# Kernel tuning notes

Hardware: AMD Instinct MI355X
Metric: run time of the kernel (lower is better)

## Reference

```python
import jax, jax.numpy as jnp
import numpy as np

NUM_USER = 100000
NUM_ITEM = 50000
DIM_E = 128
DIM_FEAT = 256
BATCH = 1024
NUM_NEG = 127
TEMP = 2.0
LR_LAMBDA = 0.5
NUM_SAMPLE = 0.5


def _l2norm(x, eps=1e-12):
    n = jnp.linalg.norm(x, axis=1, keepdims=True)
    return x / jnp.maximum(n, eps)


def setup_inputs() -> dict:
    key = jax.random.key(0)
    ks = jax.random.split(key, 9)
    flat = BATCH * (1 + NUM_NEG)
    user_tensor = jax.random.randint(ks[0], (BATCH, 1 + NUM_NEG), 0, NUM_USER, dtype=jnp.int64 if jax.config.jax_enable_x64 else jnp.int32)
    item_tensor = jax.random.randint(ks[1], (BATCH, 1 + NUM_NEG), NUM_USER, NUM_USER + NUM_ITEM, dtype=user_tensor.dtype)
    rand_index = jax.random.randint(ks[2], (int(flat * NUM_SAMPLE),), 0, flat, dtype=user_tensor.dtype)
    id_embedding = jax.random.normal(ks[3], (NUM_USER + NUM_ITEM, DIM_E), jnp.float32) * 0.02
    v_feat = jax.random.normal(ks[4], (NUM_ITEM, DIM_FEAT), jnp.float32)
    W1 = jax.random.normal(ks[5], (DIM_FEAT, 256), jnp.float32) * (1.0 / np.sqrt(DIM_FEAT))
    b1 = jax.random.normal(ks[6], (256,), jnp.float32) * 0.01
    W2 = jax.random.normal(ks[7], (256, DIM_E), jnp.float32) * (1.0 / 16.0)
    b2 = jax.random.normal(ks[8], (DIM_E,), jnp.float32) * 0.01
    return {"user_tensor": user_tensor, "item_tensor": item_tensor, "rand_index": rand_index,
            "id_embedding": id_embedding, "v_feat": v_feat, "W1": W1, "b1": b1, "W2": W2, "b2": b2}


def _contrastive(anchor, all_t):
    # exp(<a,b>/T) grouped into [B, 1+num_neg]; pos is column 0
    score = jnp.exp(jnp.sum(anchor * all_t, axis=1) / TEMP).reshape(-1, 1 + NUM_NEG)
    pos = score[:, 0]
    tot = jnp.sum(score, axis=1)
    return jnp.mean(-jnp.log(pos / tot))


def reference(user_tensor, item_tensor, rand_index, id_embedding, v_feat, W1, b1, W2, b2):
    # encoder: normalize content feats, 2-layer MLP
    feature = _l2norm(v_feat)
    feature = jax.nn.leaky_relu(feature @ W1 + b1)  # slope 0.01, matches torch default
    feature = feature @ W2 + b2                      # [num_item, dim_E]

    pos_flat = jnp.repeat(item_tensor[:, 0:1], 1 + NUM_NEG, axis=1).reshape(-1)
    u_flat = user_tensor.reshape(-1)
    i_flat = item_tensor.reshape(-1)

    all_item_feat = feature[i_flat - NUM_USER]          # [flat, dim_E]
    user_emb = id_embedding[u_flat]
    pos_emb = id_embedding[pos_flat]
    all_item_emb = id_embedding[i_flat]

    head_feat = _l2norm(all_item_feat)
    head_embed = _l2norm(pos_emb)

    # replace a random half of the item embeddings with content features
    all_item_input = all_item_emb.at[rand_index].set(all_item_feat[rand_index])

    c1 = _contrastive(head_embed, head_feat)
    c2 = _contrastive(user_emb, all_item_input)

    reg_loss = (jnp.mean(jnp.sqrt(jnp.sum(user_emb ** 2, axis=1))) +
                jnp.mean(jnp.sqrt(jnp.sum(all_item_emb ** 2, axis=1)))) / 2

    # graph_generator is None -> graph contrastive loss is 0
    total = c1 * LR_LAMBDA + c2 * (1.0 - LR_LAMBDA)
    return total, reg_loss
```

## Files before the change

kernel.cpp:

```cpp
#include <hip/hip_runtime.h>
#include <math.h>

#define NUSER 100000
#define NITEM 50000
#define NID   (NUSER + NITEM)
#define DIM_E 128
#define DIM_F 256
#define BATCH 1024
#define NCOL 128
#define FLAT (BATCH * NCOL)

typedef __attribute__((ext_vector_type(8))) short bf16x8;
typedef __attribute__((ext_vector_type(4))) short bf16x4;
typedef __attribute__((ext_vector_type(4))) float f32x4;

__device__ __forceinline__ float dot4(float4 a, float4 b) {
    return a.x * b.x + a.y * b.y + a.z * b.z + a.w * b.w;
}

__device__ __forceinline__ short f2bf(float x) {
    unsigned u = __float_as_uint(x);
    unsigned r = (u + 0x7FFFu + ((u >> 16) & 1u)) >> 16;
    return (short)r;
}

__device__ __forceinline__ float bf2f(short s) {
    return __uint_as_float(((unsigned)(unsigned short)s) << 16);
}

__global__ __launch_bounds__(256) void zero_flags_kernel(int* __restrict__ flags) {
    int i = blockIdx.x * 256 + threadIdx.x;
    if (i < FLAT) flags[i] = 0;
}

__global__ __launch_bounds__(256) void scatter_flags_kernel(const int* __restrict__ ridx,
                                                            int n, int* __restrict__ flags) {
    int i = blockIdx.x * 256 + threadIdx.x;
    if (i < n) flags[ridx[i]] = 1;
}

__global__ __launch_bounds__(256) void prep_kernel(const float* __restrict__ W1,
                                                   const float* __restrict__ W2,
                                                   short* __restrict__ w1t,
                                                   short* __restrict__ w2t) {
    int i = blockIdx.x * 256 + threadIdx.x;
    if (i < 256 * 256) {
        int n = i >> 8, k = i & 255;
        w1t[i] = f2bf(W1[(size_t)k * 256 + n]);
    } else if (i < 256 * 256 + 128 * 256) {
        int j = i - 256 * 256;
        int n = j >> 8, k = j & 255;
        w2t[j] = f2bf(W2[(size_t)k * 128 + n]);
    }
}

__global__ __launch_bounds__(256) void conv_kernel(const float* __restrict__ idemb,
                                                   short* __restrict__ idemb_bf,
                                                   float* __restrict__ norms) {
    const int sub = threadIdx.x & 31;
    const int g0 = (blockIdx.x * 256 + threadIdx.x) >> 5;
    const int ng = gridDim.x * 8;
    for (int row = g0; row < NID; row += ng) {
        float4 v = *(const float4*)(idemb + (size_t)row * DIM_E + sub * 4);
        float s = dot4(v, v);
#pragma unroll
        for (int off = 16; off >= 1; off >>= 1) s += __shfl_xor(s, off);
        bf16x4 p;
        p[0] = f2bf(v.x); p[1] = f2bf(v.y); p[2] = f2bf(v.z); p[3] = f2bf(v.w);
        *(bf16x4*)(idemb_bf + (size_t)row * DIM_E + sub * 4) = p;
        if (sub == 0) norms[row] = sqrtf(s);
    }
}

__device__ __forceinline__ void stage_rows(const float4 va[4], int srow, int q,
                                           short* __restrict__ As) {
    float s = 0.f;
#pragma unroll
    for (int c = 0; c < 4; ++c) s += dot4(va[c], va[c]);
#pragma unroll
    for (int off = 8; off >= 1; off >>= 1) s += __shfl_xor(s, off);
    float inv = 1.f / fmaxf(sqrtf(s), 1e-12f);
    bf16x8 p0, p1;
    p0[0] = f2bf(va[0].x * inv); p0[1] = f2bf(va[0].y * inv);
    p0[2] = f2bf(va[0].z * inv); p0[3] = f2bf(va[0].w * inv);
    p0[4] = f2bf(va[1].x * inv); p0[5] = f2bf(va[1].y * inv);
    p0[6] = f2bf(va[1].z * inv); p0[7] = f2bf(va[1].w * inv);
    p1[0] = f2bf(va[2].x * inv); p1[1] = f2bf(va[2].y * inv);
    p1[2] = f2bf(va[2].z * inv); p1[3] = f2bf(va[2].w * inv);
    p1[4] = f2bf(va[3].x * inv); p1[5] = f2bf(va[3].y * inv);
    p1[6] = f2bf(va[3].z * inv); p1[7] = f2bf(va[3].w * inv);
    const int sw = (srow & 7) << 3;
    *(bf16x8*)(&As[srow * 256 + ((q * 16) ^ sw)]) = p0;
    *(bf16x8*)(&As[srow * 256 + ((q * 16 + 8) ^ sw)]) = p1;
}

__global__ __launch_bounds__(512, 2) void mlp_mfma_kernel(const float* __restrict__ vfeat,
                                                          const short* __restrict__ w1t,
                                                          const float* __restrict__ b1,
                                                          const short* __restrict__ w2t,
                                                          const float* __restrict__ b2,
                                                          short* __restrict__ featout) {
    __shared__ __align__(16) short As[32 * 256];
    __shared__ __align__(16) short Hs[32 * 256];
    const int t = threadIdx.x;
    const int w = t >> 6;
    const int l = t & 63;
    const int fr = l & 15;
    const int kg = l >> 4;
    const int srow = t >> 4;
    const int q = t & 15;
    const int NT = (NITEM + 31) / 32;

    bf16x8 B1f[8][2];
    bf16x8 B2f[8];
#pragma unroll
    for (int kc = 0; kc < 8; ++kc) {
#pragma unroll
        for (int ct = 0; ct < 2; ++ct)
            B1f[kc][ct] = *(const bf16x8*)(w1t + (size_t)(w * 32 + ct * 16 + fr) * 256 + kc * 32 + kg * 8);
        B2f[kc] = *(const bf16x8*)(w2t + (size_t)(w * 16 + fr) * 256 + kc * 32 + kg * 8);
    }
    float b1v[2];
    b1v[0] = b1[w * 32 + fr];
    b1v[1] = b1[w * 32 + 16 + fr];
    const float b2v = b2[w * 16 + fr];

    int tile = blockIdx.x;
    {
        float4 va[4];
        int gr = tile * 32 + srow;
        const float* src = vfeat + (size_t)gr * DIM_F + q * 16;
#pragma unroll
        for (int c = 0; c < 4; ++c)
            va[c] = (gr < NITEM) ? *(const float4*)(src + c * 4) : make_float4(0.f, 0.f, 0.f, 0.f);
        stage_rows(va, srow, q, As);
    }
    __syncthreads();

    while (tile < NT) {
        const int tnext = tile + gridDim.x;
        float4 vb[4];
        if (tnext < NT) {
            int gr = tnext * 32 + srow;
            const float* src = vfeat + (size_t)gr * DIM_F + q * 16;
#pragma unroll
            for (int c = 0; c < 4; ++c)
                vb[c] = (gr < NITEM) ? *(const float4*)(src + c * 4) : make_float4(0.f, 0.f, 0.f, 0.f);
        }

        {
            f32x4 acc1[2][2];
#pragma unroll
            for (int rt = 0; rt < 2; ++rt)
#pragma unroll
                for (int ct = 0; ct < 2; ++ct) acc1[rt][ct] = (f32x4){0.f, 0.f, 0.f, 0.f};
#pragma unroll
            for (int kc = 0; kc < 8; ++kc) {
                const int kb = kc * 32 + kg * 8;
                bf16x8 af[2];
#pragma unroll
                for (int rt = 0; rt < 2; ++rt) {
                    int row = rt * 16 + fr;
                    af[rt] = *(const bf16x8*)(&As[row * 256 + (kb ^ ((row & 7) << 3))]);
                }
#pragma unroll
                for (int ct = 0; ct < 2; ++ct)
#pragma unroll
                    for (int rt = 0; rt < 2; ++rt)
                        acc1[rt][ct] = __builtin_amdgcn_mfma_f32_16x16x32_bf16(af[rt], B1f[kc][ct], acc1[rt][ct], 0, 0, 0);
            }
#pragma unroll
            for (int rt = 0; rt < 2; ++rt)
#pragma unroll
                for (int ct = 0; ct < 2; ++ct) {
                    int colH = w * 32 + ct * 16 + fr;
#pragma unroll
                    for (int r = 0; r < 4; ++r) {
                        float h = acc1[rt][ct][r] + b1v[ct];
                        h = h > 0.f ? h : 0.01f * h;
                        int row = rt * 16 + kg * 4 + r;
                        Hs[row * 256 + (colH ^ ((row & 7) << 3))] = f2bf(h);
                    }
                }
        }
        __syncthreads();

        {
            f32x4 acc2[2];
            acc2[0] = (f32x4){0.f, 0.f, 0.f, 0.f};
            acc2[1] = (f32x4){0.f, 0.f, 0.f, 0.f};
#pragma unroll
            for (int kc = 0; kc < 8; ++kc) {
                const int kb = kc * 32 + kg * 8;
#pragma unroll
                for (int rt = 0; rt < 2; ++rt) {
                    int row = rt * 16 + fr;
                    bf16x8 hf = *(const bf16x8*)(&Hs[row * 256 + (kb ^ ((row & 7) << 3))]);
                    acc2[rt] = __builtin_amdgcn_mfma_f32_16x16x32_bf16(hf, B2f[kc], acc2[rt], 0, 0, 0);
                }
            }
            const int col = w * 16 + fr;
#pragma unroll
            for (int rt = 0; rt < 2; ++rt)
#pragma unroll
                for (int r = 0; r < 4; ++r) {
                    int row = tile * 32 + rt * 16 + kg * 4 + r;
                    if (row < NITEM) featout[(size_t)row * DIM_E + col] = f2bf(acc2[rt][r] + b2v);
                }
        }

        if (tnext < NT) stage_rows(vb, srow, q, As);
        __syncthreads();
        tile = tnext;
    }
}

__global__ __launch_bounds__(256) void contrast_kernel(const int* __restrict__ user,
                                                       const int* __restrict__ item,
                                                       const int* __restrict__ flags,
                                                       const float* __restrict__ idemb,
                                                       const short* __restrict__ idemb_bf,
                                                       const float* __restrict__ norms,
                                                       const short* __restrict__ feat,
                                                       float* __restrict__ rowvals) {
    __shared__ float pe[128];
    __shared__ float s1s[128], s2s[128], rs[128];
    const int row = blockIdx.x;
    const int t = threadIdx.x;

    if (t < 32) {
        int p = item[(size_t)row * NCOL];
        float4 v = *(const float4*)(idemb + (size_t)p * DIM_E + t * 4);
        float s = dot4(v, v);
#pragma unroll
        for (int off = 16; off >= 1; off >>= 1) s += __shfl_xor(s, off);
        float inv = 1.f / fmaxf(sqrtf(s), 1e-12f);
        *(float4*)(&pe[t * 4]) = make_float4(v.x * inv, v.y * inv, v.z * inv, v.w * inv);
    }
    __syncthreads();

    const int e = t >> 1;
    const int h = t & 1;
    const size_t j = (size_t)row * NCOL + e;
    const int u = user[j];
    const int it = item[j];
    const int fl = flags[j];
    const short* up = idemb_bf + (size_t)u * DIM_E + h * 64;
    const short* ip = idemb_bf + (size_t)it * DIM_E + h * 64;
    const short* fp = feat + (size_t)(it - NUSER) * DIM_E + h * 64;

    bf16x8 ub[8], fb[8], xb[8];
#pragma unroll
    for (int i = 0; i < 8; ++i) { ub[i] = ((const bf16x8*)up)[i]; fb[i] = ((const bf16x8*)fp)[i]; }
    if (fl) {
#pragma unroll
        for (int i = 0; i < 8; ++i) xb[i] = fb[i];
    } else {
#pragma unroll
        for (int i = 0; i < 8; ++i) xb[i] = ((const bf16x8*)ip)[i];
    }
    float nu = norms[u];
    float ni = norms[it];

    float sf = 0.f, dpf = 0.f, dux = 0.f;
#pragma unroll
    for (int i = 0; i < 8; ++i) {
        float4 p0 = *(const float4*)(&pe[h * 64 + i * 8]);
        float4 p1 = *(const float4*)(&pe[h * 64 + i * 8 + 4]);
        float pk[8] = {p0.x, p0.y, p0.z, p0.w, p1.x, p1.y, p1.z, p1.w};
#pragma unroll
        for (int k = 0; k < 8; ++k) {
            float fv = bf2f(fb[i][k]);
            float uv = bf2f(ub[i][k]);
            float xv = bf2f(xb[i][k]);
            sf += fv * fv;
            dpf += pk[k] * fv;
            dux += uv * xv;
        }
    }
    sf += __shfl_xor(sf, 1);
    dpf += __shfl_xor(dpf, 1);
    dux += __shfl_xor(dux, 1);

    if (h == 0) {
        float fnorm = fmaxf(sqrtf(sf), 1e-12f);
        s1s[e] = expf(dpf / fnorm * 0.5f);
        s2s[e] = expf(dux * 0.5f);
        rs[e] = nu + ni;
    }
    __syncthreads();

    if (t < 64) {
        float a1 = s1s[t] + s1s[t + 64];
        float a2 = s2s[t] + s2s[t + 64];
        float a3 = rs[t] + rs[t + 64];
#pragma unroll
        for (int off = 32; off >= 1; off >>= 1) {
            a1 += __shfl_xor(a1, off);
            a2 += __shfl_xor(a2, off);
            a3 += __shfl_xor(a3, off);
        }
        if (t == 0) {
            rowvals[row * 4 + 0] = logf(a1) - logf(s1s[0]);
            rowvals[row * 4 + 1] = logf(a2) - logf(s2s[0]);
            rowvals[row * 4 + 2] = a3;
        }
    }
}

__global__ __launch_bounds__(256) void finalize_kernel(const float* __restrict__ rowvals,
                                                       float* __restrict__ out) {
    float c1 = 0.f, c2 = 0.f, rg = 0.f;
    for (int i = threadIdx.x; i < BATCH; i += 256) {
        c1 += rowvals[i * 4 + 0];
        c2 += rowvals[i * 4 + 1];
        rg += rowvals[i * 4 + 2];
    }
#pragma unroll
    for (int off = 32; off >= 1; off >>= 1) {
        c1 += __shfl_xor(c1, off);
        c2 += __shfl_xor(c2, off);
        rg += __shfl_xor(rg, off);
    }
    __shared__ float buf[4][3];
    int wid = threadIdx.x >> 6, lane = threadIdx.x & 63;
    if (lane == 0) { buf[wid][0] = c1; buf[wid][1] = c2; buf[wid][2] = rg; }
    __syncthreads();
    if (threadIdx.x == 0) {
        float C1 = buf[0][0] + buf[1][0] + buf[2][0] + buf[3][0];
        float C2 = buf[0][1] + buf[1][1] + buf[2][1] + buf[3][1];
        float R  = buf[0][2] + buf[1][2] + buf[2][2] + buf[3][2];
        out[0] = 0.5f * (C1 / (float)BATCH) + 0.5f * (C2 / (float)BATCH);
        out[1] = 0.5f * (R / (float)FLAT);
    }
}

extern "C" void kernel_launch(void* const* d_in, const int* in_sizes, int n_in,
                              void* d_out, int out_size, void* d_ws, size_t ws_size,
                              hipStream_t stream) {
    const int* user = (const int*)d_in[0];
    const int* item = (const int*)d_in[1];
    const int* ridx = (const int*)d_in[2];
    const float* idemb = (const float*)d_in[3];
    const float* vfeat = (const float*)d_in[4];
    const float* W1 = (const float*)d_in[5];
    const float* b1 = (const float*)d_in[6];
    const float* W2 = (const float*)d_in[7];
    const float* b2 = (const float*)d_in[8];
    float* out = (float*)d_out;

    char* ws = (char*)d_ws;
    short* feat_bf  = (short*)(ws);
    short* idemb_bf = (short*)(ws + 12800000);
    float* norms    = (float*)(ws + 51200000);
    int*   flags    = (int*)  (ws + 51800000);
    float* rowvals  = (float*)(ws + 52324288);
    short* w1t      = (short*)(ws + 52340672);
    short* w2t      = (short*)(ws + 52471744);

    const int nridx = in_sizes[2];

    conv_kernel<<<dim3(2048), dim3(256), 0, stream>>>(idemb, idemb_bf, norms);
    prep_kernel<<<dim3(384), dim3(256), 0, stream>>>(W1, W2, w1t, w2t);
    zero_flags_kernel<<<dim3((FLAT + 255) / 256), dim3(256), 0, stream>>>(flags);
    scatter_flags_kernel<<<dim3((nridx + 255) / 256), dim3(256), 0, stream>>>(ridx, nridx, flags);
    mlp_mfma_kernel<<<dim3(256), dim3(512), 0, stream>>>(vfeat, w1t, b1, w2t, b2, feat_bf);
    contrast_kernel<<<dim3(BATCH), dim3(256), 0, stream>>>(user, item, flags, idemb, idemb_bf, norms, feat_bf, rowvals);
    finalize_kernel<<<dim3(1), dim3(256), 0, stream>>>(rowvals, out);
}
```

Measured before the change: 79.06 us.

## Fuse prep kernels, co-schedule embedding conversion with MLP, split contrast rows

Merges flag zeroing with weight transposition, and folds flag scatter plus id-embedding bf16 conversion into extra blocks of the MLP kernel so they run concurrently with the MFMA tiles. The launch count drops from seven to four. Each contrast row is split across two 128-thread blocks, with the log-sum-exp combined in finalize using stored positive logits. This targets launch overhead and idle CUs during the serial prep stages, at the cost of more partial-result traffic and blocks competing for resources inside the fused kernel.

Measured after the change: 77.97 us. About the same (-1.4%).

```diff
diff --git a/kernel.cpp b/kernel.cpp
--- a/kernel.cpp
+++ b/kernel.cpp
@@ -28,22 +28,13 @@
     return __uint_as_float(((unsigned)(unsigned short)s) << 16);
 }
 
-__global__ __launch_bounds__(256) void zero_flags_kernel(int* __restrict__ flags) {
+__global__ __launch_bounds__(256) void prep0_kernel(const float* __restrict__ W1,
+                                                    const float* __restrict__ W2,
+                                                    short* __restrict__ w1t,
+                                                    short* __restrict__ w2t,
+                                                    int* __restrict__ flags) {
     int i = blockIdx.x * 256 + threadIdx.x;
     if (i < FLAT) flags[i] = 0;
-}
-
-__global__ __launch_bounds__(256) void scatter_flags_kernel(const int* __restrict__ ridx,
-                                                            int n, int* __restrict__ flags) {
-    int i = blockIdx.x * 256 + threadIdx.x;
-    if (i < n) flags[ridx[i]] = 1;
-}
-
-__global__ __launch_bounds__(256) void prep_kernel(const float* __restrict__ W1,
-                                                   const float* __restrict__ W2,
-                                                   short* __restrict__ w1t,
-                                                   short* __restrict__ w2t) {
-    int i = blockIdx.x * 256 + threadIdx.x;
     if (i < 256 * 256) {
         int n = i >> 8, k = i & 255;
         w1t[i] = f2bf(W1[(size_t)k * 256 + n]);
@@ -51,24 +42,6 @@
         int j = i - 256 * 256;
         int n = j >> 8, k = j & 255;
         w2t[j] = f2bf(W2[(size_t)k * 128 + n]);
-    }
-}
-
-__global__ __launch_bounds__(256) void conv_kernel(const float* __restrict__ idemb,
-                                                   short* __restrict__ idemb_bf,
-                                                   float* __restrict__ norms) {
-    const int sub = threadIdx.x & 31;
-    const int g0 = (blockIdx.x * 256 + threadIdx.x) >> 5;
-    const int ng = gridDim.x * 8;
-    for (int row = g0; row < NID; row += ng) {
-        float4 v = *(const float4*)(idemb + (size_t)row * DIM_E + sub * 4);
-        float s = dot4(v, v);
-#pragma unroll
-        for (int off = 16; off >= 1; off >>= 1) s += __shfl_xor(s, off);
-        bf16x4 p;
-        p[0] = f2bf(v.x); p[1] = f2bf(v.y); p[2] = f2bf(v.z); p[3] = f2bf(v.w);
-        *(bf16x4*)(idemb_bf + (size_t)row * DIM_E + sub * 4) = p;
-        if (sub == 0) norms[row] = sqrtf(s);
     }
 }
 
@@ -94,15 +67,42 @@
     *(bf16x8*)(&As[srow * 256 + ((q * 16 + 8) ^ sw)]) = p1;
 }
 
-__global__ __launch_bounds__(512, 2) void mlp_mfma_kernel(const float* __restrict__ vfeat,
-                                                          const short* __restrict__ w1t,
-                                                          const float* __restrict__ b1,
-                                                          const short* __restrict__ w2t,
-                                                          const float* __restrict__ b2,
-                                                          short* __restrict__ featout) {
+__global__ __launch_bounds__(512, 2) void fused_prep_kernel(const float* __restrict__ vfeat,
+                                                            const short* __restrict__ w1t,
+                                                            const float* __restrict__ b1,
+                                                            const short* __restrict__ w2t,
+                                                            const float* __restrict__ b2,
+                                                            short* __restrict__ featout,
+                                                            const float* __restrict__ idemb,
+                                                            short* __restrict__ idemb_bf,
+                                                            float* __restrict__ norms,
+                                                            const int* __restrict__ ridx,
+                                                            int nridx,
+                                                            int* __restrict__ flags) {
     __shared__ __align__(16) short As[32 * 256];
     __shared__ __align__(16) short Hs[32 * 256];
     const int t = threadIdx.x;
+
+    if (blockIdx.x >= 256) {
+        const int blk = blockIdx.x - 256;
+        if (blk < 128) {
+            for (int i = blk * 512 + t; i < nridx; i += 128 * 512) flags[ridx[i]] = 1;
+        }
+        const int sub = t & 31;
+        int row = blk * 16 + (t >> 5);
+        for (; row < NID; row += 768 * 16) {
+            float4 v = *(const float4*)(idemb + (size_t)row * DIM_E + sub * 4);
+            float s = dot4(v, v);
+#pragma unroll
+            for (int off = 16; off >= 1; off >>= 1) s += __shfl_xor(s, off);
+            bf16x4 p;
+            p[0] = f2bf(v.x); p[1] = f2bf(v.y); p[2] = f2bf(v.z); p[3] = f2bf(v.w);
+            *(bf16x4*)(idemb_bf + (size_t)row * DIM_E + sub * 4) = p;
+            if (sub == 0) norms[row] = sqrtf(s);
+        }
+        return;
+    }
+
     const int w = t >> 6;
     const int l = t & 63;
     const int fr = l & 15;
@@ -138,7 +138,7 @@
     __syncthreads();
 
     while (tile < NT) {
-        const int tnext = tile + gridDim.x;
+        const int tnext = tile + 256;
         float4 vb[4];
         if (tnext < NT) {
             int gr = tnext * 32 + srow;
@@ -215,17 +215,19 @@
     }
 }
 
-__global__ __launch_bounds__(256) void contrast_kernel(const int* __restrict__ user,
+__global__ __launch_bounds__(128) void contrast_kernel(const int* __restrict__ user,
                                                        const int* __restrict__ item,
                                                        const int* __restrict__ flags,
                                                        const float* __restrict__ idemb,
                                                        const short* __restrict__ idemb_bf,
                                                        const float* __restrict__ norms,
                                                        const short* __restrict__ feat,
-                                                       float* __restrict__ rowvals) {
+                                                       float* __restrict__ rowpart) {
     __shared__ float pe[128];
-    __shared__ float s1s[128], s2s[128], rs[128];
-    const int row = blockIdx.x;
+    __shared__ float s1s[64], s2s[64], rs[64];
+    __shared__ float dpos[2];
+    const int row = blockIdx.x >> 1;
+    const int part = blockIdx.x & 1;
     const int t = threadIdx.x;
 
     if (t < 32) {
@@ -239,7 +241,8 @@
     }
     __syncthreads();
 
-    const int e = t >> 1;
+    const int el = t >> 1;
+    const int e = part * 64 + el;
     const int h = t & 1;
     const size_t j = (size_t)row * NCOL + e;
     const int u = user[j];
@@ -284,37 +287,46 @@
 
     if (h == 0) {
         float fnorm = fmaxf(sqrtf(sf), 1e-12f);
-        s1s[e] = expf(dpf / fnorm * 0.5f);
-        s2s[e] = expf(dux * 0.5f);
-        rs[e] = nu + ni;
+        float d1 = dpf / fnorm * 0.5f;
+        float d2 = dux * 0.5f;
+        s1s[el] = expf(d1);
+        s2s[el] = expf(d2);
+        rs[el] = nu + ni;
+        if (e == 0) { dpos[0] = d1; dpos[1] = d2; }
     }
     __syncthreads();
 
-    if (t < 64) {
-        float a1 = s1s[t] + s1s[t + 64];
-        float a2 = s2s[t] + s2s[t + 64];
-        float a3 = rs[t] + rs[t + 64];
-#pragma unroll
-        for (int off = 32; off >= 1; off >>= 1) {
+    if (t < 32) {
+        float a1 = s1s[t] + s1s[t + 32];
+        float a2 = s2s[t] + s2s[t + 32];
+        float a3 = rs[t] + rs[t + 32];
+#pragma unroll
+        for (int off = 16; off >= 1; off >>= 1) {
             a1 += __shfl_xor(a1, off);
             a2 += __shfl_xor(a2, off);
             a3 += __shfl_xor(a3, off);
         }
         if (t == 0) {
-            rowvals[row * 4 + 0] = logf(a1) - logf(s1s[0]);
-            rowvals[row * 4 + 1] = logf(a2) - logf(s2s[0]);
-            rowvals[row * 4 + 2] = a3;
-        }
-    }
-}
-
-__global__ __launch_bounds__(256) void finalize_kernel(const float* __restrict__ rowvals,
+            float* dst = rowpart + (size_t)blockIdx.x * 6;
+            dst[0] = a1;
+            dst[1] = a2;
+            dst[2] = a3;
+            if (part == 0) { dst[3] = dpos[0]; dst[4] = dpos[1]; }
+        }
+    }
+}
+
+__global__ __launch_bounds__(256) void finalize_kernel(const float* __restrict__ rowpart,
                                                        float* __restrict__ out) {
     float c1 = 0.f, c2 = 0.f, rg = 0.f;
-    for (int i = threadIdx.x; i < BATCH; i += 256) {
-        c1 += rowvals[i * 4 + 0];
-        c2 += rowvals[i * 4 + 1];
-        rg += rowvals[i * 4 + 2];
+    for (int r = threadIdx.x; r < BATCH; r += 256) {
+        const float* p0 = rowpart + (size_t)(r * 2) * 6;
+        const float* p1 = rowpart + (size_t)(r * 2 + 1) * 6;
+        float A1 = p0[0] + p1[0];
+        float A2 = p0[1] + p1[1];
+        c1 += logf(A1) - p0[3];
+        c2 += logf(A2) - p0[4];
+        rg += p0[2] + p1[2];
     }
 #pragma unroll
     for (int off = 32; off >= 1; off >>= 1) {
@@ -354,17 +366,17 @@
     short* idemb_bf = (short*)(ws + 12800000);
     float* norms    = (float*)(ws + 51200000);
     int*   flags    = (int*)  (ws + 51800000);
-    float* rowvals  = (float*)(ws + 52324288);
-    short* w1t      = (short*)(ws + 52340672);
-    short* w2t      = (short*)(ws + 52471744);
+    float* rowpart  = (float*)(ws + 52324288);
+    short* w1t      = (short*)(ws + 52373440);
+    short* w2t      = (short*)(ws + 52504512);
 
     const int nridx = in_sizes[2];
 
-    conv_kernel<<<dim3(2048), dim3(256), 0, stream>>>(idemb, idemb_bf, norms);
-    prep_kernel<<<dim3(384), dim3(256), 0, stream>>>(W1, W2, w1t, w2t);
-    zero_flags_kernel<<<dim3((FLAT + 255) / 256), dim3(256), 0, stream>>>(flags);
-    scatter_flags_kernel<<<dim3((nridx + 255) / 256), dim3(256), 0, stream>>>(ridx, nridx, flags);
-    mlp_mfma_kernel<<<dim3(256), dim3(512), 0, stream>>>(vfeat, w1t, b1, w2t, b2, feat_bf);
-    contrast_kernel<<<dim3(BATCH), dim3(256), 0, stream>>>(user, item, flags, idemb, idemb_bf, norms, feat_bf, rowvals);
-    finalize_kernel<<<dim3(1), dim3(256), 0, stream>>>(rowvals, out);
-}
+    prep0_kernel<<<dim3(512), dim3(256), 0, stream>>>(W1, W2, w1t, w2t, flags);
+    fused_prep_kernel<<<dim3(1024), dim3(512), 0, stream>>>(vfeat, w1t, b1, w2t, b2, feat_bf,
+                                                            idemb, idemb_bf, norms,
+                                                            ridx, nridx, flags);
+    contrast_kernel<<<dim3(2 * BATCH), dim3(128), 0, stream>>>(user, item, flags, idemb,
+                                                               idemb_bf, norms, feat_bf, rowpart);
+    finalize_kernel<<<dim3(1), dim3(256), 0, stream>>>(rowpart, out);
+}
```
